# Optimization experiments

Measured on AMD Instinct MI355X. Metric: run time of the kernel, lower is better.

Reference implementation:

```python
import jax, jax.numpy as jnp
import numpy as np

B, S, IN_DIM, OUT_DIM = 8, 8192, 1024, 1024


def setup_inputs() -> dict:
    key = jax.random.key(0)
    k1, k2, k3, k4 = jax.random.split(key, 4)
    x = jax.random.normal(k1, (B, S, IN_DIM), dtype=jnp.float32)
    visual_mask = jax.random.randint(k2, (B, S), 0, 2) == 1  # bool [B,S]
    # nn.Linear weights are [out_dim, in_dim]
    w_v = jax.random.normal(k3, (OUT_DIM, IN_DIM), dtype=jnp.float32) * (IN_DIM ** -0.5)
    w_t = jax.random.normal(k4, (OUT_DIM, IN_DIM), dtype=jnp.float32) * (IN_DIM ** -0.5)
    return {"x": x, "visual_mask": visual_mask, "w_v": w_v, "w_t": w_t}


def reference(x, visual_mask, w_v, w_t):
    # Per-token routed dual linear: out[b,s] = x[b,s] @ (w_v if mask else w_t).T
    out_v = jnp.einsum("bsi,oi->bso", x, w_v)  # [B,S,OUT]
    out_t = jnp.einsum("bsi,oi->bso", x, w_t)  # [B,S,OUT]
    return jnp.where(visual_mask[:, :, None], out_v, out_t)
```

## Files before the change

kernel.cpp:

```cpp
#include <hip/hip_runtime.h>
#include <stdint.h>

#define TOKENS 65536
#define KDIM 1024
#define NDIM 1024
#define MROWS 65792
#define ROWTILES 257
#define NTILES 4
#define NWG (ROWTILES * NTILES)
#define BK 64
#define NT 16

using short8 = __attribute__((ext_vector_type(8))) short;
using f32x4  = __attribute__((ext_vector_type(4))) float;

#define ASYNC_COPY16(g, l) __builtin_amdgcn_global_load_lds( \
    (const __attribute__((address_space(1))) void*)(g),      \
    (__attribute__((address_space(3))) void*)(l), 16, 0, 0)

__device__ __forceinline__ short f2bf(float f) {
    union { float f; unsigned u; } c; c.f = f;
    unsigned r = c.u + 0x7FFFu + ((c.u >> 16) & 1u);
    return (short)(r >> 16);
}

__global__ __launch_bounds__(256) void detect_mask_fmt(const unsigned* __restrict__ mask,
                                                       int* __restrict__ hdr) {
    int i = blockIdx.x * 256 + threadIdx.x;
    unsigned w = mask[i];
    int mode = 0;
    if (w == 0x3F800000u)      mode = 2;
    else if (w > 1u)           mode = 1;
    if (mode) atomicMax(&hdr[2], mode);
}

__device__ __forceinline__ bool read_mask(const void* mask, int fmt, int t) {
    if (fmt == 2) return ((const float*)mask)[t] != 0.0f;
    if (fmt == 1) return ((const unsigned char*)mask)[t] != 0;
    return ((const int*)mask)[t] != 0;
}

__global__ __launch_bounds__(256) void route_assign(const void* __restrict__ mask,
                                                    int* __restrict__ rowmap,
                                                    int* __restrict__ slotmap,
                                                    int* __restrict__ hdr) {
    const int tid  = threadIdx.x;
    const int lane = tid & 63;
    const int wid  = tid >> 6;
    const int t    = blockIdx.x * 256 + tid;
    const int fmt  = hdr[2];
    const bool m   = read_mask(mask, fmt, t);

    unsigned long long bal = __ballot(m);
    int vpre = __popcll(bal & ((1ull << lane) - 1ull));
    int vcnt = __popcll(bal);
    int tpre = lane - vpre;
    int tcnt = 64 - vcnt;

    __shared__ int cv[4], ct[4], ov[4], ot[4];
    __shared__ int bv, bt;
    if (lane == 0) { cv[wid] = vcnt; ct[wid] = tcnt; }
    __syncthreads();
    if (tid == 0) {
        int sv = 0, st = 0;
        for (int w = 0; w < 4; ++w) { ov[w] = sv; sv += cv[w]; ot[w] = st; st += ct[w]; }
        bv = atomicAdd(&hdr[0], sv);
        bt = atomicAdd(&hdr[1], st);
    }
    __syncthreads();
    int slot = m ? (bv + ov[wid] + vpre)
                 : (MROWS - 1 - (bt + ot[wid] + tpre));
    rowmap[slot] = t;
    slotmap[t] = slot;
}

__global__ __launch_bounds__(256) void gather_convert(const float* __restrict__ x,
                                                      const int* __restrict__ slotmap,
                                                      short* __restrict__ Abuf) {
    const int lane = threadIdx.x & 63;
    const int t    = blockIdx.x * 4 + (threadIdx.x >> 6);
    const int slot = slotmap[t];
    const float* src = x + (size_t)t * KDIM;
    short* dst = Abuf + (size_t)slot * KDIM;
#pragma unroll
    for (int p = 0; p < 4; ++p) {
        int k = p * 256 + lane * 4;
        float4 v = *(const float4*)(src + k);
        short4 o;
        o.x = f2bf(v.x); o.y = f2bf(v.y); o.z = f2bf(v.z); o.w = f2bf(v.w);
        *(short4*)(dst + k) = o;
    }
}

__global__ __launch_bounds__(256) void convert_weights(const float* __restrict__ wv,
                                                       const float* __restrict__ wt,
                                                       short* __restrict__ ovp,
                                                       short* __restrict__ otp) {
    int i = (blockIdx.x * 256 + threadIdx.x) * 4;
    const float* src; short* dst; int off;
    if (i < NDIM * KDIM) { src = wv; dst = ovp; off = i; }
    else                 { src = wt; dst = otp; off = i - NDIM * KDIM; }
    float4 v = *(const float4*)(src + off);
    short4 o;
    o.x = f2bf(v.x); o.y = f2bf(v.y); o.z = f2bf(v.z); o.w = f2bf(v.w);
    *(short4*)(dst + off) = o;
}


#define QUAD(MB, NB)                                                              \
    do {                                                                          \
        _Pragma("unroll") for (int m_ = 0; m_ < 4; ++m_)                          \
        _Pragma("unroll") for (int n_ = 0; n_ < 2; ++n_)                          \
        _Pragma("unroll") for (int ks_ = 0; ks_ < 2; ++ks_)                       \
            acc[(MB) + m_][(NB) + n_] = __builtin_amdgcn_mfma_f32_16x16x32_bf16(  \
                a[2 * m_ + ks_], b[2 * ((NB) + n_) + ks_],                        \
                acc[(MB) + m_][(NB) + n_], 0, 0, 0);                              \
    } while (0)

template<bool STAGE, int ENDM>
__device__ __forceinline__ void kstep(const char* pA, const char* pB,
                                      char* lA, char* lB,
                                      const short* aS, const short* bS,
                                      f32x4 (&acc)[8][4], int xorhi) {
    short8 a[8], b[8];
#pragma unroll
    for (int m = 0; m < 4; ++m) {
        a[2*m]   = *(const short8*)(pA + m * 2048 + (0  ^ xorhi));
        a[2*m+1] = *(const short8*)(pA + m * 2048 + (64 ^ xorhi));
    }
#pragma unroll
    for (int n = 0; n < 4; ++n) {
        b[2*n]   = *(const short8*)(pB + n * 2048 + (0  ^ xorhi));
        b[2*n+1] = *(const short8*)(pB + n * 2048 + (64 ^ xorhi));
    }
    __builtin_amdgcn_s_barrier();
    asm volatile("s_waitcnt lgkmcnt(0)" ::: "memory");
    __builtin_amdgcn_sched_barrier(0);
    __builtin_amdgcn_s_setprio(1);
    QUAD(0, 0);
    __builtin_amdgcn_s_setprio(0);
    __builtin_amdgcn_s_barrier();
    if (STAGE) {
        ASYNC_COPY16(bS,                     lB);
        ASYNC_COPY16(bS + (size_t)64 * KDIM, lB + 8192);
    }
    __builtin_amdgcn_s_barrier();
    __builtin_amdgcn_s_setprio(1);
    QUAD(0, 2);
    __builtin_amdgcn_s_setprio(0);
    __builtin_amdgcn_s_barrier();
#pragma unroll
    for (int m = 0; m < 4; ++m) {
        a[2*m]   = *(const short8*)(pA + (4 + m) * 2048 + (0  ^ xorhi));
        a[2*m+1] = *(const short8*)(pA + (4 + m) * 2048 + (64 ^ xorhi));
    }
    if (STAGE) {
        ASYNC_COPY16(bS + (size_t)128 * KDIM, lB + 16384);
        ASYNC_COPY16(bS + (size_t)192 * KDIM, lB + 16384 + 8192);
    }
    __builtin_amdgcn_s_barrier();
    asm volatile("s_waitcnt lgkmcnt(0)" ::: "memory");
    __builtin_amdgcn_sched_barrier(0);
    __builtin_amdgcn_s_setprio(1);
    QUAD(4, 0);
    __builtin_amdgcn_s_setprio(0);
    __builtin_amdgcn_s_barrier();
    if (STAGE) {
        ASYNC_COPY16(aS,                      lA);
        ASYNC_COPY16(aS + (size_t)64  * KDIM, lA + 8192);
        ASYNC_COPY16(aS + (size_t)128 * KDIM, lA + 16384);
        ASYNC_COPY16(aS + (size_t)192 * KDIM, lA + 16384 + 8192);
    }
    __builtin_amdgcn_s_barrier();
    __builtin_amdgcn_s_setprio(1);
    QUAD(4, 2);
    __builtin_amdgcn_s_setprio(0);
    if (ENDM == 0) asm volatile("s_waitcnt vmcnt(8)" ::: "memory");
    if (ENDM == 1) asm volatile("s_waitcnt vmcnt(0)" ::: "memory");
    if (ENDM < 2)  __builtin_amdgcn_s_barrier();
}

__device__ __forceinline__ void stage_ktile(char* lA, char* lB,
                                            const short* aS, const short* bS) {
    ASYNC_COPY16(aS,                      lA);
    ASYNC_COPY16(aS + (size_t)64  * KDIM, lA + 8192);
    ASYNC_COPY16(aS + (size_t)128 * KDIM, lA + 16384);
    ASYNC_COPY16(aS + (size_t)192 * KDIM, lA + 16384 + 8192);
    ASYNC_COPY16(bS,                      lB);
    ASYNC_COPY16(bS + (size_t)64  * KDIM, lB + 8192);
    ASYNC_COPY16(bS + (size_t)128 * KDIM, lB + 16384);
    ASYNC_COPY16(bS + (size_t)192 * KDIM, lB + 16384 + 8192);
}

__global__ __launch_bounds__(512, 2) void gemm_routed(const short* __restrict__ Abuf,
                                                      const short* __restrict__ Wv,
                                                      const short* __restrict__ Wt,
                                                      const int* __restrict__ rowmap,
                                                      const int* __restrict__ hdr,
                                                      float* __restrict__ out) {
    __shared__ __align__(16) short As[2 * 256 * 64];
    __shared__ __align__(16) short Bs[2 * 256 * 64];
    __shared__ int rmap_s[256];

    const int q = NWG / 8, r = NWG % 8;
    const int xcd = blockIdx.x & 7, ii = blockIdx.x >> 3;
    const int wgid = (xcd < r ? xcd * (q + 1) : r * (q + 1) + (xcd - r) * q) + ii;
    const int r0 = (wgid >> 2) * 256;
    const int n0 = (wgid & 3) * 256;

    const int Mv = hdr[0];
    if (r0 == Mv) return;
    const short* Wsel = (r0 < Mv) ? Wv : Wt;

    const int tid  = threadIdx.x;
    const int lane = tid & 63;
    const int wvid = tid >> 6;
    const int wr   = wvid >> 2;
    const int wc   = wvid & 3;

    if (tid < 256) rmap_s[tid] = rowmap[r0 + tid];

    const int arow = tid >> 3;
    const int achk = (tid & 7) ^ (arow & 7);
    const short* aSrc = Abuf + (size_t)(r0 + arow) * KDIM + achk * 8;
    const short* bSrc = Wsel + (size_t)(n0 + arow) * KDIM + achk * 8;
    char* lA0 = (char*)As + wvid * 1024;
    char* lB0 = (char*)Bs + wvid * 1024;
    char* lA1 = lA0 + 32768;
    char* lB1 = lB0 + 32768;

    const int xorhi = (lane & 4) << 4;
    const char* aRd = (const char*)As + wr * 16384 + (lane & 15) * 128
                      + (((lane >> 4) * 16) ^ ((lane & 3) << 4));
    const char* bRd = (const char*)Bs + (wc >> 1) * 16384
                      + (((wc & 1) * 64 + (lane & 15)) * 128)
                      + (((lane >> 4) * 16) ^ ((lane & 3) << 4));
    const char* pA0 = aRd;       const char* pA1 = aRd + 32768;
    const char* pB0 = bRd;       const char* pB1 = bRd + 32768;

    f32x4 acc[8][4];
#pragma unroll
    for (int m = 0; m < 8; ++m)
#pragma unroll
        for (int n = 0; n < 4; ++n) acc[m][n] = f32x4{0.f, 0.f, 0.f, 0.f};

    stage_ktile(lA0, lB0, aSrc + 0 * BK, bSrc + 0 * BK);
    stage_ktile(lA1, lB1, aSrc + 1 * BK, bSrc + 1 * BK);
    asm volatile("s_waitcnt vmcnt(8)" ::: "memory");
    __builtin_amdgcn_s_barrier();

    for (int it = 0; it < 7; ++it) {
        const int k2 = 2 * it + 2, k3 = 2 * it + 3;
        kstep<true, 0>(pA0, pB0, lA0, lB0, aSrc + k2 * BK, bSrc + k2 * BK, acc, xorhi);
        kstep<true, 0>(pA1, pB1, lA1, lB1, aSrc + k3 * BK, bSrc + k3 * BK, acc, xorhi);
    }
    kstep<false, 1>(pA0, pB0, lA0, lB0, aSrc, bSrc, acc, xorhi);
    kstep<false, 2>(pA1, pB1, lA1, lB1, aSrc, bSrc, acc, xorhi);

    const int colbase = n0 + wc * 64 + (lane & 15);
#pragma unroll
    for (int m = 0; m < 8; ++m) {
        const int rb = wr * 128 + m * 16 + ((lane >> 4) << 2);
#pragma unroll
        for (int i2 = 0; i2 < 4; ++i2) {
            int token = rmap_s[rb + i2];
            if (token < 0) continue;
            float* orow = out + (size_t)token * NDIM + colbase;
            orow[0]  = acc[m][0][i2];
            orow[16] = acc[m][1][i2];
            orow[32] = acc[m][2][i2];
            orow[48] = acc[m][3][i2];
        }
    }
}

__global__ __launch_bounds__(256) void fallback_matvec(const float* __restrict__ x,
                                                       const void* __restrict__ mask,
                                                       const float* __restrict__ wv,
                                                       const float* __restrict__ wt,
                                                       const int* __restrict__ hdr,
                                                       float* __restrict__ out) {
    __shared__ float xs[KDIM];
    const int t = blockIdx.x;
    const int fmt = hdr[2];
    const bool m = read_mask(mask, fmt, t);
    const float* w = m ? wv : wt;
    const float* src = x + (size_t)t * KDIM;
    for (int k = threadIdx.x; k < KDIM; k += 256) xs[k] = src[k];
    __syncthreads();
    for (int n = threadIdx.x; n < NDIM; n += 256) {
        const float* wr = w + (size_t)n * KDIM;
        float s = 0.f;
        for (int k = 0; k < KDIM; ++k) s += xs[k] * wr[k];
        out[(size_t)t * NDIM + n] = s;
    }
}

extern "C" void kernel_launch(void* const* d_in, const int* in_sizes, int n_in,
                              void* d_out, int out_size, void* d_ws, size_t ws_size,
                              hipStream_t stream) {
    const float* x    = (const float*)d_in[0];
    const void*  mask = d_in[1];
    const float* w_v  = (const float*)d_in[2];
    const float* w_t  = (const float*)d_in[3];
    float* out = (float*)d_out;

    char* ws = (char*)d_ws;
    int*   hdr     = (int*)ws;
    int*   rowmap  = (int*)(ws + 4096);
    int*   slotmap = (int*)(ws + 270336);
    short* wvb     = (short*)(ws + 532480);
    short* wtb     = (short*)(ws + 2629632);
    short* Abuf    = (short*)(ws + 4726784);
    const size_t need = 4726784ull + (size_t)MROWS * KDIM * sizeof(short);

    if (ws_size >= need) {
        hipMemsetAsync(hdr, 0, 16, stream);
        hipMemsetAsync(rowmap, 0xFF, MROWS * sizeof(int), stream);
        detect_mask_fmt<<<64, 256, 0, stream>>>((const unsigned*)mask, hdr);
        route_assign<<<TOKENS / 256, 256, 0, stream>>>(mask, rowmap, slotmap, hdr);
        gather_convert<<<TOKENS / 4, 256, 0, stream>>>(x, slotmap, Abuf);
        convert_weights<<<(2 * NDIM * KDIM) / (256 * 4), 256, 0, stream>>>(w_v, w_t, wvb, wtb);
        gemm_routed<<<NWG, 512, 0, stream>>>(Abuf, wvb, wtb, rowmap, hdr, out);
    } else {
        hipMemsetAsync(hdr, 0, 16, stream);
        detect_mask_fmt<<<64, 256, 0, stream>>>((const unsigned*)mask, hdr);
        fallback_matvec<<<TOKENS, 256, 0, stream>>>(x, mask, w_v, w_t, hdr, out);
    }
}
```

Before: 653.9 us.

## Fuse token gather and bf16 conversion into GEMM A-tile loading

```diff
diff --git a/kernel.cpp b/kernel.cpp
--- a/kernel.cpp
+++ b/kernel.cpp
@@ -9,7 +9,6 @@
 #define NTILES 4
 #define NWG (ROWTILES * NTILES)
 #define BK 64
-#define NT 16
 
 using short8 = __attribute__((ext_vector_type(8))) short;
 using f32x4  = __attribute__((ext_vector_type(4))) float;
@@ -42,7 +41,6 @@
 
 __global__ __launch_bounds__(256) void route_assign(const void* __restrict__ mask,
                                                     int* __restrict__ rowmap,
-                                                    int* __restrict__ slotmap,
                                                     int* __restrict__ hdr) {
     const int tid  = threadIdx.x;
     const int lane = tid & 63;
@@ -71,25 +69,6 @@
     int slot = m ? (bv + ov[wid] + vpre)
                  : (MROWS - 1 - (bt + ot[wid] + tpre));
     rowmap[slot] = t;
-    slotmap[t] = slot;
-}
-
-__global__ __launch_bounds__(256) void gather_convert(const float* __restrict__ x,
-                                                      const int* __restrict__ slotmap,
-                                                      short* __restrict__ Abuf) {
-    const int lane = threadIdx.x & 63;
-    const int t    = blockIdx.x * 4 + (threadIdx.x >> 6);
-    const int slot = slotmap[t];
-    const float* src = x + (size_t)t * KDIM;
-    short* dst = Abuf + (size_t)slot * KDIM;
-#pragma unroll
-    for (int p = 0; p < 4; ++p) {
-        int k = p * 256 + lane * 4;
-        float4 v = *(const float4*)(src + k);
-        short4 o;
-        o.x = f2bf(v.x); o.y = f2bf(v.y); o.z = f2bf(v.z); o.w = f2bf(v.w);
-        *(short4*)(dst + k) = o;
-    }
 }
 
 __global__ __launch_bounds__(256) void convert_weights(const float* __restrict__ wv,
@@ -117,16 +96,32 @@
                 acc[(MB) + m_][(NB) + n_], 0, 0, 0);                              \
     } while (0)
 
-template<bool STAGE, int ENDM>
-__device__ __forceinline__ void kstep(const char* pA, const char* pB,
-                                      char* lA, char* lB,
-                                      const short* aS, const short* bS,
+__device__ __forceinline__ void wbA(char* dst, const float4 (&ast)[8]) {
+#pragma unroll
+    for (int q = 0; q < 4; ++q) {
+        short8 o;
+        o[0] = f2bf(ast[2*q].x);   o[1] = f2bf(ast[2*q].y);
+        o[2] = f2bf(ast[2*q].z);   o[3] = f2bf(ast[2*q].w);
+        o[4] = f2bf(ast[2*q+1].x); o[5] = f2bf(ast[2*q+1].y);
+        o[6] = f2bf(ast[2*q+1].z); o[7] = f2bf(ast[2*q+1].w);
+        *(short8*)(dst + q * 256) = o;
+    }
+}
+
+template<bool ISSUE, int ENDM>
+__device__ __forceinline__ void kstep(const char* pA, const char* pB, char* lB, char* aWB,
+                                      const float* xrow, int kf2, const short* bS2,
                                       f32x4 (&acc)[8][4], int xorhi) {
     short8 a[8], b[8];
+    float4 ast[8];
+    if (ISSUE) {
+#pragma unroll
+        for (int i = 0; i < 8; ++i) ast[i] = *(const float4*)(xrow + kf2 + 4 * i);
+    }
 #pragma unroll
     for (int m = 0; m < 4; ++m) {
-        a[2*m]   = *(const short8*)(pA + m * 2048 + (0  ^ xorhi));
-        a[2*m+1] = *(const short8*)(pA + m * 2048 + (64 ^ xorhi));
+        a[2*m]   = *(const short8*)(pA + (2*m)     * 1024);
+        a[2*m+1] = *(const short8*)(pA + (2*m + 1) * 1024);
     }
 #pragma unroll
     for (int n = 0; n < 4; ++n) {
@@ -136,63 +131,41 @@
     __builtin_amdgcn_s_barrier();
     asm volatile("s_waitcnt lgkmcnt(0)" ::: "memory");
     __builtin_amdgcn_sched_barrier(0);
-    __builtin_amdgcn_s_setprio(1);
-    QUAD(0, 0);
-    __builtin_amdgcn_s_setprio(0);
-    __builtin_amdgcn_s_barrier();
-    if (STAGE) {
-        ASYNC_COPY16(bS,                     lB);
-        ASYNC_COPY16(bS + (size_t)64 * KDIM, lB + 8192);
-    }
-    __builtin_amdgcn_s_barrier();
-    __builtin_amdgcn_s_setprio(1);
-    QUAD(0, 2);
-    __builtin_amdgcn_s_setprio(0);
+    __builtin_amdgcn_s_setprio(1);  QUAD(0, 0);  __builtin_amdgcn_s_setprio(0);
+    __builtin_amdgcn_s_barrier();
+    if (ISSUE) {
+        ASYNC_COPY16(bS2,                     lB);
+        ASYNC_COPY16(bS2 + (size_t)64 * KDIM, lB + 8192);
+    }
+    __builtin_amdgcn_s_setprio(1);  QUAD(0, 2);  __builtin_amdgcn_s_setprio(0);
     __builtin_amdgcn_s_barrier();
 #pragma unroll
     for (int m = 0; m < 4; ++m) {
-        a[2*m]   = *(const short8*)(pA + (4 + m) * 2048 + (0  ^ xorhi));
-        a[2*m+1] = *(const short8*)(pA + (4 + m) * 2048 + (64 ^ xorhi));
-    }
-    if (STAGE) {
-        ASYNC_COPY16(bS + (size_t)128 * KDIM, lB + 16384);
-        ASYNC_COPY16(bS + (size_t)192 * KDIM, lB + 16384 + 8192);
+        a[2*m]   = *(const short8*)(pA + (8 + 2*m) * 1024);
+        a[2*m+1] = *(const short8*)(pA + (9 + 2*m) * 1024);
+    }
+    if (ISSUE) {
+        ASYNC_COPY16(bS2 + (size_t)128 * KDIM, lB + 16384);
+        ASYNC_COPY16(bS2 + (size_t)192 * KDIM, lB + 16384 + 8192);
     }
     __builtin_amdgcn_s_barrier();
     asm volatile("s_waitcnt lgkmcnt(0)" ::: "memory");
     __builtin_amdgcn_sched_barrier(0);
-    __builtin_amdgcn_s_setprio(1);
-    QUAD(4, 0);
-    __builtin_amdgcn_s_setprio(0);
-    __builtin_amdgcn_s_barrier();
-    if (STAGE) {
-        ASYNC_COPY16(aS,                      lA);
-        ASYNC_COPY16(aS + (size_t)64  * KDIM, lA + 8192);
-        ASYNC_COPY16(aS + (size_t)128 * KDIM, lA + 16384);
-        ASYNC_COPY16(aS + (size_t)192 * KDIM, lA + 16384 + 8192);
-    }
-    __builtin_amdgcn_s_barrier();
-    __builtin_amdgcn_s_setprio(1);
-    QUAD(4, 2);
-    __builtin_amdgcn_s_setprio(0);
-    if (ENDM == 0) asm volatile("s_waitcnt vmcnt(8)" ::: "memory");
-    if (ENDM == 1) asm volatile("s_waitcnt vmcnt(0)" ::: "memory");
-    if (ENDM < 2)  __builtin_amdgcn_s_barrier();
-}
-
-__device__ __forceinline__ void stage_ktile(char* lA, char* lB,
-                                            const short* aS, const short* bS) {
-    ASYNC_COPY16(aS,                      lA);
-    ASYNC_COPY16(aS + (size_t)64  * KDIM, lA + 8192);
-    ASYNC_COPY16(aS + (size_t)128 * KDIM, lA + 16384);
-    ASYNC_COPY16(aS + (size_t)192 * KDIM, lA + 16384 + 8192);
-    ASYNC_COPY16(bS,                      lB);
-    ASYNC_COPY16(bS + (size_t)64  * KDIM, lB + 8192);
-    ASYNC_COPY16(bS + (size_t)128 * KDIM, lB + 16384);
-    ASYNC_COPY16(bS + (size_t)192 * KDIM, lB + 16384 + 8192);
-}
-
-__global__ __launch_bounds__(512, 2) void gemm_routed(const short* __restrict__ Abuf,
+    __builtin_amdgcn_s_setprio(1);  QUAD(4, 0);  __builtin_amdgcn_s_setprio(0);
+    __builtin_amdgcn_s_barrier();
+    __builtin_amdgcn_s_setprio(1);  QUAD(4, 2);  __builtin_amdgcn_s_setprio(0);
+    if (ENDM == 0) {
+        asm volatile("s_waitcnt vmcnt(4)" ::: "memory");
+        wbA(aWB, ast);
+        asm volatile("s_waitcnt lgkmcnt(0)" ::: "memory");
+        __builtin_amdgcn_s_barrier();
+    } else if (ENDM == 1) {
+        asm volatile("s_waitcnt vmcnt(0)" ::: "memory");
+        __builtin_amdgcn_s_barrier();
+    }
+}
+
+__global__ __launch_bounds__(512, 2) void gemm_routed(const float* __restrict__ x,
                                                       const short* __restrict__ Wv,
                                                       const short* __restrict__ Wt,
                                                       const int* __restrict__ rowmap,
@@ -219,24 +192,28 @@
     const int wc   = wvid & 3;
 
     if (tid < 256) rmap_s[tid] = rowmap[r0 + tid];
-
-    const int arow = tid >> 3;
-    const int achk = (tid & 7) ^ (arow & 7);
-    const short* aSrc = Abuf + (size_t)(r0 + arow) * KDIM + achk * 8;
-    const short* bSrc = Wsel + (size_t)(n0 + arow) * KDIM + achk * 8;
-    char* lA0 = (char*)As + wvid * 1024;
+    __syncthreads();
+
+    const int arow = tid >> 1, ahalf = tid & 1;
+    int tok = rmap_s[arow]; if (tok < 0) tok = 0;
+    const float* xrow = x + (size_t)tok * KDIM + ahalf * 32;
+    char* aWB0 = (char*)As + ((arow >> 4) * 2 + ahalf) * 1024 + (arow & 15) * 16;
+    char* aWB1 = aWB0 + 32768;
+
+    const int brow = tid >> 3;
+    const int bchk = (tid & 7) ^ (brow & 7);
+    const short* bSrc = Wsel + (size_t)(n0 + brow) * KDIM + bchk * 8;
     char* lB0 = (char*)Bs + wvid * 1024;
-    char* lA1 = lA0 + 32768;
     char* lB1 = lB0 + 32768;
 
     const int xorhi = (lane & 4) << 4;
-    const char* aRd = (const char*)As + wr * 16384 + (lane & 15) * 128
-                      + (((lane >> 4) * 16) ^ ((lane & 3) << 4));
+    const char* pA0 = (const char*)As + wr * 16384 + lane * 16;
+    const char* pA1 = pA0 + 32768;
     const char* bRd = (const char*)Bs + (wc >> 1) * 16384
                       + (((wc & 1) * 64 + (lane & 15)) * 128)
                       + (((lane >> 4) * 16) ^ ((lane & 3) << 4));
-    const char* pA0 = aRd;       const char* pA1 = aRd + 32768;
-    const char* pB0 = bRd;       const char* pB1 = bRd + 32768;
+    const char* pB0 = bRd;
+    const char* pB1 = bRd + 32768;
 
     f32x4 acc[8][4];
 #pragma unroll
@@ -244,18 +221,34 @@
 #pragma unroll
         for (int n = 0; n < 4; ++n) acc[m][n] = f32x4{0.f, 0.f, 0.f, 0.f};
 
-    stage_ktile(lA0, lB0, aSrc + 0 * BK, bSrc + 0 * BK);
-    stage_ktile(lA1, lB1, aSrc + 1 * BK, bSrc + 1 * BK);
-    asm volatile("s_waitcnt vmcnt(8)" ::: "memory");
-    __builtin_amdgcn_s_barrier();
-
-    for (int it = 0; it < 7; ++it) {
-        const int k2 = 2 * it + 2, k3 = 2 * it + 3;
-        kstep<true, 0>(pA0, pB0, lA0, lB0, aSrc + k2 * BK, bSrc + k2 * BK, acc, xorhi);
-        kstep<true, 0>(pA1, pB1, lA1, lB1, aSrc + k3 * BK, bSrc + k3 * BK, acc, xorhi);
-    }
-    kstep<false, 1>(pA0, pB0, lA0, lB0, aSrc, bSrc, acc, xorhi);
-    kstep<false, 2>(pA1, pB1, lA1, lB1, aSrc, bSrc, acc, xorhi);
+    {
+        float4 ast[8];
+#pragma unroll
+        for (int i = 0; i < 8; ++i) ast[i] = *(const float4*)(xrow + 0 * BK + 4 * i);
+        ASYNC_COPY16(bSrc + 0 * BK,                     lB0);
+        ASYNC_COPY16(bSrc + 0 * BK + (size_t)64 * KDIM, lB0 + 8192);
+        ASYNC_COPY16(bSrc + 0 * BK + (size_t)128 * KDIM, lB0 + 16384);
+        ASYNC_COPY16(bSrc + 0 * BK + (size_t)192 * KDIM, lB0 + 16384 + 8192);
+        ASYNC_COPY16(bSrc + 1 * BK,                     lB1);
+        ASYNC_COPY16(bSrc + 1 * BK + (size_t)64 * KDIM, lB1 + 8192);
+        ASYNC_COPY16(bSrc + 1 * BK + (size_t)128 * KDIM, lB1 + 16384);
+        ASYNC_COPY16(bSrc + 1 * BK + (size_t)192 * KDIM, lB1 + 16384 + 8192);
+        wbA(aWB0, ast);
+#pragma unroll
+        for (int i = 0; i < 8; ++i) ast[i] = *(const float4*)(xrow + 1 * BK + 4 * i);
+        wbA(aWB1, ast);
+        asm volatile("s_waitcnt vmcnt(0) lgkmcnt(0)" ::: "memory");
+        __builtin_amdgcn_s_barrier();
+    }
+
+    kstep<true, 0>(pA0, pB0, lB0, aWB0, xrow,  2 * BK, bSrc + (size_t)2 * BK, acc, xorhi);
+    for (int it = 0; it < 6; ++it) {
+        kstep<true, 0>(pA1, pB1, lB1, aWB1, xrow, (2*it+3) * BK, bSrc + (size_t)(2*it+3) * BK, acc, xorhi);
+        kstep<true, 0>(pA0, pB0, lB0, aWB0, xrow, (2*it+4) * BK, bSrc + (size_t)(2*it+4) * BK, acc, xorhi);
+    }
+    kstep<true, 0>(pA1, pB1, lB1, aWB1, xrow, 15 * BK, bSrc + (size_t)15 * BK, acc, xorhi);
+    kstep<false, 1>(pA0, pB0, lB0, aWB0, xrow, 0, bSrc, acc, xorhi);
+    kstep<false, 2>(pA1, pB1, lB1, aWB1, xrow, 0, bSrc, acc, xorhi);
 
     const int colbase = n0 + wc * 64 + (lane & 15);
 #pragma unroll
@@ -308,20 +301,17 @@
     char* ws = (char*)d_ws;
     int*   hdr     = (int*)ws;
     int*   rowmap  = (int*)(ws + 4096);
-    int*   slotmap = (int*)(ws + 270336);
     short* wvb     = (short*)(ws + 532480);
     short* wtb     = (short*)(ws + 2629632);
-    short* Abuf    = (short*)(ws + 4726784);
-    const size_t need = 4726784ull + (size_t)MROWS * KDIM * sizeof(short);
+    const size_t need = 4726784ull;
 
     if (ws_size >= need) {
         hipMemsetAsync(hdr, 0, 16, stream);
         hipMemsetAsync(rowmap, 0xFF, MROWS * sizeof(int), stream);
         detect_mask_fmt<<<64, 256, 0, stream>>>((const unsigned*)mask, hdr);
-        route_assign<<<TOKENS / 256, 256, 0, stream>>>(mask, rowmap, slotmap, hdr);
-        gather_convert<<<TOKENS / 4, 256, 0, stream>>>(x, slotmap, Abuf);
+        route_assign<<<TOKENS / 256, 256, 0, stream>>>(mask, rowmap, hdr);
         convert_weights<<<(2 * NDIM * KDIM) / (256 * 4), 256, 0, stream>>>(w_v, w_t, wvb, wtb);
-        gemm_routed<<<NWG, 512, 0, stream>>>(Abuf, wvb, wtb, rowmap, hdr, out);
+        gemm_routed<<<NWG, 512, 0, stream>>>(x, wvb, wtb, rowmap, hdr, out);
     } else {
         hipMemsetAsync(hdr, 0, 16, stream);
         detect_mask_fmt<<<64, 256, 0, stream>>>((const unsigned*)mask, hdr);
```

Measured after the change: 717.4 us. 9.7% more time.
